# Performance work log

Hardware: AMD Instinct MI355X
Metric: run time of the kernel (lower is better)

The kernel has to match this reference:

```python
import jax, jax.numpy as jnp
import numpy as np

C = 64
EPS = 1e-5

def _layernorm(x, w, b):
    mu = jnp.mean(x, axis=-1, keepdims=True)
    var = jnp.var(x, axis=-1, keepdims=True)
    return (x - mu) * jax.lax.rsqrt(var + EPS) * w + b

def setup_inputs() -> dict:
    key = jax.random.key(0)
    ks = jax.random.split(key, 12)
    B, H, W = 4, 64, 64
    s = 1.0 / np.sqrt(C)
    inp = {
        'seg':   jax.random.normal(ks[0], (B, C, H, W), jnp.float32),
        'gauss': jax.random.normal(ks[1], (B, C, H, W), jnp.float32),
        'Wq': jax.random.normal(ks[2], (C, C), jnp.float32) * s,
        'bq': jnp.zeros((C,), jnp.float32),
        'Wk': jax.random.normal(ks[3], (C, C), jnp.float32) * s,
        'bk': jnp.zeros((C,), jnp.float32),
        'Wv': jax.random.normal(ks[4], (C, C), jnp.float32) * s,
        'bv': jnp.zeros((C,), jnp.float32),
        'ln1_w': jnp.ones((C,), jnp.float32),
        'ln1_b': jnp.zeros((C,), jnp.float32),
        'ln2_w': jnp.ones((C,), jnp.float32),
        'ln2_b': jnp.zeros((C,), jnp.float32),
        'W1': jax.random.normal(ks[5], (C, C), jnp.float32) * s,
        'b1': jnp.zeros((C,), jnp.float32),
        'W2': jax.random.normal(ks[6], (C, C), jnp.float32) * s,
        'b2': jnp.zeros((C,), jnp.float32),
    }
    return inp

def reference(seg, gauss, Wq, bq, Wk, bk, Wv, bv, ln1_w, ln1_b, ln2_w, ln2_b, W1, b1, W2, b2):
    B, Cc, H, W_ = seg.shape
    N = H * W_
    # 1x1 convs == per-pixel linear over channels; go straight to token layout
    seg_t = seg.reshape(B, Cc, N)      # [B,C,N]
    gau_t = gauss.reshape(B, Cc, N)
    q = jnp.einsum('bcn,oc->bno', seg_t, Wq) + bq        # [B,N,C]
    k = jnp.einsum('bcn,oc->bon', seg_t, Wk) + bk[None, :, None]  # [B,C,N]
    v = jnp.einsum('bcn,oc->bno', gau_t, Wv) + bv        # [B,N,C]
    scale = 1.0 / jnp.sqrt(jnp.float32(Cc))
    attn = jax.nn.softmax(jnp.einsum('bnc,bcm->bnm', q, k) * scale, axis=-1)  # [B,N,N]
    out = jnp.einsum('bnm,bmc->bnc', attn, v)
    x = _layernorm(v + out, ln1_w, ln1_b)
    ffn = jnp.einsum('bnc,oc->bno', jax.nn.relu(jnp.einsum('bnc,oc->bno', x, W1) + b1), W2) + b2
    x = _layernorm(x + ffn, ln2_w, ln2_b)
    return x.transpose(0, 2, 1).reshape(B, Cc, H, W_)
```

## Files before the change

kernel.cpp:

```cpp
#include <hip/hip_runtime.h>
#include <hip/hip_bf16.h>

typedef unsigned short u16;
typedef unsigned int u32;
typedef __attribute__((ext_vector_type(8))) short bf16x8;
typedef __attribute__((ext_vector_type(4))) float f32x4;

#define NTOK 4096
#define QSCALE2 0.18033688f

__device__ __forceinline__ float b2f(u16 u) {
    u32 v = ((u32)u) << 16;
    return __builtin_bit_cast(float, v);
}
__device__ __forceinline__ u16 f2b(float f) {
    u32 u = __builtin_bit_cast(u32, f);
    u32 r = (u + 0x7fffu + ((u >> 16) & 1u)) >> 16;
    return (u16)r;
}
__device__ __forceinline__ u32 pack2(float lo, float hi) {
    return (u32)f2b(lo) | ((u32)f2b(hi) << 16);
}
__device__ __forceinline__ u32 pk2(float lo, float hi) {
    float2 t; t.x = lo; t.y = hi;
    __hip_bfloat162 b = __float22bfloat162_rn(t);
    u32 r;
    __builtin_memcpy(&r, &b, 4);
    return r;
}
__device__ __forceinline__ bf16x8 cvt8(const float* __restrict__ p) {
    float4 a = *(const float4*)p;
    float4 b = *(const float4*)(p + 4);
    bf16x8 r;
    r[0] = (short)f2b(a.x); r[1] = (short)f2b(a.y);
    r[2] = (short)f2b(a.z); r[3] = (short)f2b(a.w);
    r[4] = (short)f2b(b.x); r[5] = (short)f2b(b.y);
    r[6] = (short)f2b(b.z); r[7] = (short)f2b(b.w);
    return r;
}

__global__ __launch_bounds__(512) void qkv_kernel(
    const float* __restrict__ seg, const float* __restrict__ gau,
    const float* __restrict__ Wq, const float* __restrict__ bq,
    const float* __restrict__ Wk, const float* __restrict__ bk,
    const float* __restrict__ Wv, const float* __restrict__ bv,
    u16* __restrict__ Qt, u16* __restrict__ Kt,
    u16* __restrict__ Vtok, u16* __restrict__ Vswz)
{
    __shared__ __align__(16) u16 sSegT[64 * 64];
    __shared__ __align__(16) u16 sGauT[64 * 64];
    const int tid = threadIdx.x;
    const int bid = blockIdx.x;
    const int xcd = bid & 7;
    const int b = xcd >> 1;
    const int nb = ((bid >> 3) << 1) | (xcd & 1);
    const int n0 = nb * 64;

    for (int idx = tid; idx < 4096; idx += 512) {
        int c = idx >> 6, t = idx & 63;
        int sw = t * 64 + ((((c >> 3) ^ (t & 7)) << 3) | (c & 7));
        sSegT[sw] = f2b(seg[(size_t)(b * 64 + c) * NTOK + n0 + t]);
        sGauT[sw] = f2b(gau[(size_t)(b * 64 + c) * NTOK + n0 + t]);
    }
    __syncthreads();

    const int lane = tid & 63;
    const int wv = tid >> 6;
    const int tb = wv & 3;
    const int task = wv >> 2;
    const int q = lane & 15, g = lane >> 4;
    const int tok = tb * 16 + q;

    const size_t obase = (size_t)b * NTOK * 64;
    const size_t rowb = (size_t)(n0 + tb * 16 + g * 4);

    if (task == 0) {
        bf16x8 as[2];
#pragma unroll
        for (int ks = 0; ks < 2; ++ks) {
            int c0 = ks * 32 + g * 8;
            int sw = tok * 64 + (((c0 >> 3) ^ (tok & 7)) << 3);
            as[ks] = *(const bf16x8*)&sSegT[sw];
        }
#pragma unroll
        for (int ob = 0; ob < 4; ++ob) {
            int o = ob * 16 + q;
            {
                float bias = bq[o];
                f32x4 acc = {bias, bias, bias, bias};
                bf16x8 w0 = cvt8(&Wq[o * 64 + g * 8]);
                bf16x8 w1 = cvt8(&Wq[o * 64 + 32 + g * 8]);
                acc = __builtin_amdgcn_mfma_f32_16x16x32_bf16(as[0], w0, acc, 0, 0, 0);
                acc = __builtin_amdgcn_mfma_f32_16x16x32_bf16(as[1], w1, acc, 0, 0, 0);
#pragma unroll
                for (int j = 0; j < 4; ++j)
                    Qt[obase + (rowb + j) * 64 + o] = f2b(acc[j] * QSCALE2);
            }
            {
                float bias = bk[o];
                f32x4 acc = {bias, bias, bias, bias};
                bf16x8 w0 = cvt8(&Wk[o * 64 + g * 8]);
                bf16x8 w1 = cvt8(&Wk[o * 64 + 32 + g * 8]);
                acc = __builtin_amdgcn_mfma_f32_16x16x32_bf16(as[0], w0, acc, 0, 0, 0);
                acc = __builtin_amdgcn_mfma_f32_16x16x32_bf16(as[1], w1, acc, 0, 0, 0);
#pragma unroll
                for (int j = 0; j < 4; ++j)
                    Kt[obase + (rowb + j) * 64 + o] = f2b(acc[j]);
            }
        }
    } else {
        bf16x8 ag[2];
#pragma unroll
        for (int ks = 0; ks < 2; ++ks) {
            int c0 = ks * 32 + g * 8;
            int sw = tok * 64 + (((c0 >> 3) ^ (tok & 7)) << 3);
            ag[ks] = *(const bf16x8*)&sGauT[sw];
        }
        const int kbg = (n0 >> 5) + (tb >> 1);
        const int half = tb & 1;
#pragma unroll
        for (int ob = 0; ob < 4; ++ob) {
            int o = ob * 16 + q;
            float bias = bv[o];
            f32x4 acc = {bias, bias, bias, bias};
            bf16x8 w0 = cvt8(&Wv[o * 64 + g * 8]);
            bf16x8 w1 = cvt8(&Wv[o * 64 + 32 + g * 8]);
            acc = __builtin_amdgcn_mfma_f32_16x16x32_bf16(ag[0], w0, acc, 0, 0, 0);
            acc = __builtin_amdgcn_mfma_f32_16x16x32_bf16(ag[1], w1, acc, 0, 0, 0);
            ushort4 v4;
            v4.x = f2b(acc[0]); v4.y = f2b(acc[1]);
            v4.z = f2b(acc[2]); v4.w = f2b(acc[3]);
#pragma unroll
            for (int j = 0; j < 4; ++j)
                Vtok[obase + (rowb + j) * 64 + o] = f2b(acc[j]);
            *(ushort4*)&Vswz[(((size_t)(b * 128 + kbg)) * 4 + ob) * 512 + lane * 8 + half * 4] = v4;
        }
    }
}

__global__ __launch_bounds__(512, 4) void attn_kernel(
    const u16* __restrict__ Qt, const u16* __restrict__ Kt,
    const u16* __restrict__ Vtok, const u16* __restrict__ Vswz,
    const float* __restrict__ ln1w, const float* __restrict__ ln1b,
    const float* __restrict__ ln2w, const float* __restrict__ ln2b,
    const float* __restrict__ W1, const float* __restrict__ b1,
    const float* __restrict__ W2, const float* __restrict__ b2,
    float* __restrict__ out)
{
    __shared__ __align__(16) float sAcc[4][32][68];
    __shared__ float sL[8][32];
    __shared__ __align__(16) u16 sX[2 * 16 * 64];

    const int tid = threadIdx.x;
    const int wv = tid >> 6;
    const int lane = tid & 63;
    const int q = lane & 15, g = lane >> 4;
    const int bid = blockIdx.x;
    const int xcd = bid & 7;
    const int b = xcd >> 1;
    const int qb = ((bid >> 3) << 1) | (xcd & 1);
    const int q0 = qb * 32;
    const size_t tb_ = (size_t)b * NTOK * 64;

    const int n_qa = q0 + q, n_qb = q0 + 16 + q;
    bf16x8 qa0 = *(const bf16x8*)&Qt[tb_ + (size_t)n_qa * 64 + g * 8];
    bf16x8 qa1 = *(const bf16x8*)&Qt[tb_ + (size_t)n_qa * 64 + 32 + g * 8];
    bf16x8 qb0 = *(const bf16x8*)&Qt[tb_ + (size_t)n_qb * 64 + g * 8];
    bf16x8 qb1 = *(const bf16x8*)&Qt[tb_ + (size_t)n_qb * 64 + 32 + g * 8];

    f32x4 zero4 = {0.f, 0.f, 0.f, 0.f};
    f32x4 acc_a[4], acc_b[4];
#pragma unroll
    for (int i = 0; i < 4; ++i) { acc_a[i] = zero4; acc_b[i] = zero4; }
    float l_a = 0.f, l_b = 0.f;

    const int kbeg = wv * 512;
    const u16* Kp = &Kt[tb_ + (size_t)kbeg * 64];
    const u16* Vsw = Vswz + ((size_t)(b * 128 + (kbeg >> 5)) * 4) * 512 + lane * 8;

    for (int kk = 0; kk < 512; kk += 32) {
        bf16x8 kf00 = *(const bf16x8*)&Kp[q * 64 + g * 8];
        bf16x8 kf01 = *(const bf16x8*)&Kp[q * 64 + 32 + g * 8];
        bf16x8 kf10 = *(const bf16x8*)&Kp[(16 + q) * 64 + g * 8];
        bf16x8 kf11 = *(const bf16x8*)&Kp[(16 + q) * 64 + 32 + g * 8];
        Kp += 32 * 64;

        const u16* vt = Vsw + (size_t)(kk >> 5) * 4 * 512;
        bf16x8 vf0 = *(const bf16x8*)&vt[0 * 512];
        bf16x8 vf1 = *(const bf16x8*)&vt[1 * 512];
        bf16x8 vf2 = *(const bf16x8*)&vt[2 * 512];
        bf16x8 vf3 = *(const bf16x8*)&vt[3 * 512];

        f32x4 s0a = __builtin_amdgcn_mfma_f32_16x16x32_bf16(kf00, qa0, zero4, 0, 0, 0);
        s0a = __builtin_amdgcn_mfma_f32_16x16x32_bf16(kf01, qa1, s0a, 0, 0, 0);
        f32x4 s1a = __builtin_amdgcn_mfma_f32_16x16x32_bf16(kf10, qa0, zero4, 0, 0, 0);
        s1a = __builtin_amdgcn_mfma_f32_16x16x32_bf16(kf11, qa1, s1a, 0, 0, 0);
        f32x4 s0b = __builtin_amdgcn_mfma_f32_16x16x32_bf16(kf00, qb0, zero4, 0, 0, 0);
        s0b = __builtin_amdgcn_mfma_f32_16x16x32_bf16(kf01, qb1, s0b, 0, 0, 0);
        f32x4 s1b = __builtin_amdgcn_mfma_f32_16x16x32_bf16(kf10, qb0, zero4, 0, 0, 0);
        s1b = __builtin_amdgcn_mfma_f32_16x16x32_bf16(kf11, qb1, s1b, 0, 0, 0);

        {
            float p0 = __builtin_exp2f(s0a[0]);
            float p1 = __builtin_exp2f(s0a[1]);
            float p2 = __builtin_exp2f(s0a[2]);
            float p3 = __builtin_exp2f(s0a[3]);
            float p4 = __builtin_exp2f(s1a[0]);
            float p5 = __builtin_exp2f(s1a[1]);
            float p6 = __builtin_exp2f(s1a[2]);
            float p7 = __builtin_exp2f(s1a[3]);
            l_a += ((p0 + p1) + (p2 + p3)) + ((p4 + p5) + (p6 + p7));
            u32 pwv[4] = {pk2(p0, p1), pk2(p2, p3), pk2(p4, p5), pk2(p6, p7)};
            bf16x8 pf = __builtin_bit_cast(bf16x8, *(const bf16x8*)pwv);
            acc_a[0] = __builtin_amdgcn_mfma_f32_16x16x32_bf16(vf0, pf, acc_a[0], 0, 0, 0);
            acc_a[1] = __builtin_amdgcn_mfma_f32_16x16x32_bf16(vf1, pf, acc_a[1], 0, 0, 0);
            acc_a[2] = __builtin_amdgcn_mfma_f32_16x16x32_bf16(vf2, pf, acc_a[2], 0, 0, 0);
            acc_a[3] = __builtin_amdgcn_mfma_f32_16x16x32_bf16(vf3, pf, acc_a[3], 0, 0, 0);
        }
        {
            float p0 = __builtin_exp2f(s0b[0]);
            float p1 = __builtin_exp2f(s0b[1]);
            float p2 = __builtin_exp2f(s0b[2]);
            float p3 = __builtin_exp2f(s0b[3]);
            float p4 = __builtin_exp2f(s1b[0]);
            float p5 = __builtin_exp2f(s1b[1]);
            float p6 = __builtin_exp2f(s1b[2]);
            float p7 = __builtin_exp2f(s1b[3]);
            l_b += ((p0 + p1) + (p2 + p3)) + ((p4 + p5) + (p6 + p7));
            u32 pwv[4] = {pk2(p0, p1), pk2(p2, p3), pk2(p4, p5), pk2(p6, p7)};
            bf16x8 pf = __builtin_bit_cast(bf16x8, *(const bf16x8*)pwv);
            acc_b[0] = __builtin_amdgcn_mfma_f32_16x16x32_bf16(vf0, pf, acc_b[0], 0, 0, 0);
            acc_b[1] = __builtin_amdgcn_mfma_f32_16x16x32_bf16(vf1, pf, acc_b[1], 0, 0, 0);
            acc_b[2] = __builtin_amdgcn_mfma_f32_16x16x32_bf16(vf2, pf, acc_b[2], 0, 0, 0);
            acc_b[3] = __builtin_amdgcn_mfma_f32_16x16x32_bf16(vf3, pf, acc_b[3], 0, 0, 0);
        }
    }

    l_a += __shfl_xor(l_a, 16); l_a += __shfl_xor(l_a, 32);
    l_b += __shfl_xor(l_b, 16); l_b += __shfl_xor(l_b, 32);

    if (wv >= 4) {
        const int s = wv - 4;
        sL[wv][q] = l_a;      sL[wv][16 + q] = l_b;
#pragma unroll
        for (int cb = 0; cb < 4; ++cb) {
            *(f32x4*)&sAcc[s][q][cb * 16 + g * 4] = acc_a[cb];
            *(f32x4*)&sAcc[s][16 + q][cb * 16 + g * 4] = acc_b[cb];
        }
    }
    __syncthreads();

    if (wv < 4) {
        l_a += sL[wv + 4][q];
        l_b += sL[wv + 4][16 + q];
#pragma unroll
        for (int cb = 0; cb < 4; ++cb) {
            f32x4 pa = *(const f32x4*)&sAcc[wv][q][cb * 16 + g * 4];
            f32x4 pb = *(const f32x4*)&sAcc[wv][16 + q][cb * 16 + g * 4];
#pragma unroll
            for (int j = 0; j < 4; ++j) {
                acc_a[cb][j] += pa[j];
                acc_b[cb][j] += pb[j];
            }
        }
        sL[wv][q] = l_a;      sL[wv][16 + q] = l_b;
#pragma unroll
        for (int cb = 0; cb < 4; ++cb) {
            *(f32x4*)&sAcc[wv][q][cb * 16 + g * 4] = acc_a[cb];
            *(f32x4*)&sAcc[wv][16 + q][cb * 16 + g * 4] = acc_b[cb];
        }
    }
    __syncthreads();
    if (wv >= 2) return;

    const int qe = wv * 16 + q;
    const int n_q = q0 + qe;

    float L = sL[0][qe] + sL[1][qe] + sL[2][qe] + sL[3][qe];
    f32x4 o[4];
#pragma unroll
    for (int cb = 0; cb < 4; ++cb) o[cb] = zero4;
#pragma unroll
    for (int w = 0; w < 4; ++w) {
#pragma unroll
        for (int cb = 0; cb < 4; ++cb) {
            f32x4 aw = *(const f32x4*)&sAcc[w][qe][cb * 16 + g * 4];
#pragma unroll
            for (int j = 0; j < 4; ++j) o[cb][j] += aw[j];
        }
    }

    float inv_l = 1.0f / L;
    float x1[4][4];
#pragma unroll
    for (int cb = 0; cb < 4; ++cb) {
        ushort4 vv = *(const ushort4*)&Vtok[tb_ + (size_t)n_q * 64 + cb * 16 + g * 4];
        x1[cb][0] = o[cb][0] * inv_l + b2f(vv.x);
        x1[cb][1] = o[cb][1] * inv_l + b2f(vv.y);
        x1[cb][2] = o[cb][2] * inv_l + b2f(vv.z);
        x1[cb][3] = o[cb][3] * inv_l + b2f(vv.w);
    }

    float s_ = 0.f;
#pragma unroll
    for (int cb = 0; cb < 4; ++cb)
        for (int j = 0; j < 4; ++j) s_ += x1[cb][j];
    s_ += __shfl_xor(s_, 16); s_ += __shfl_xor(s_, 32);
    float mean = s_ * (1.f / 64.f);
    float v_ = 0.f;
#pragma unroll
    for (int cb = 0; cb < 4; ++cb)
        for (int j = 0; j < 4; ++j) { float d = x1[cb][j] - mean; v_ += d * d; }
    v_ += __shfl_xor(v_, 16); v_ += __shfl_xor(v_, 32);
    float rstd = rsqrtf(v_ * (1.f / 64.f) + 1e-5f);

    float xh[4][4];
#pragma unroll
    for (int cb = 0; cb < 4; ++cb) {
        float4 lw = *(const float4*)&ln1w[cb * 16 + g * 4];
        float4 lb = *(const float4*)&ln1b[cb * 16 + g * 4];
        xh[cb][0] = (x1[cb][0] - mean) * rstd * lw.x + lb.x;
        xh[cb][1] = (x1[cb][1] - mean) * rstd * lw.y + lb.y;
        xh[cb][2] = (x1[cb][2] - mean) * rstd * lw.z + lb.z;
        xh[cb][3] = (x1[cb][3] - mean) * rstd * lw.w + lb.w;
    }

    u32* sXu = (u32*)sX;
    const int xwr = wv * 512 + q * 32;
#pragma unroll
    for (int cb = 0; cb < 4; ++cb) {
        sXu[xwr + cb * 8 + g * 2 + 0] = pack2(xh[cb][0], xh[cb][1]);
        sXu[xwr + cb * 8 + g * 2 + 1] = pack2(xh[cb][2], xh[cb][3]);
    }
    asm volatile("s_waitcnt lgkmcnt(0)" ::: "memory");
    __builtin_amdgcn_sched_barrier(0);
    const u16* xrp = &sX[wv * 1024 + q * 64 + g * 8];
    bf16x8 xb0 = *(const bf16x8*)&xrp[0];
    bf16x8 xb1 = *(const bf16x8*)&xrp[32];

    float h[4][4];
#pragma unroll
    for (int ob = 0; ob < 4; ++ob) {
        float4 bb = *(const float4*)&b1[ob * 16 + g * 4];
        f32x4 hacc = {bb.x, bb.y, bb.z, bb.w};
        bf16x8 w0 = cvt8(&W1[(size_t)(ob * 16 + q) * 64 + g * 8]);
        bf16x8 w1 = cvt8(&W1[(size_t)(ob * 16 + q) * 64 + 32 + g * 8]);
        hacc = __builtin_amdgcn_mfma_f32_16x16x32_bf16(w0, xb0, hacc, 0, 0, 0);
        hacc = __builtin_amdgcn_mfma_f32_16x16x32_bf16(w1, xb1, hacc, 0, 0, 0);
#pragma unroll
        for (int j = 0; j < 4; ++j) h[ob][j] = fmaxf(hacc[j], 0.f);
    }

#pragma unroll
    for (int ob = 0; ob < 4; ++ob) {
        sXu[xwr + ob * 8 + g * 2 + 0] = pack2(h[ob][0], h[ob][1]);
        sXu[xwr + ob * 8 + g * 2 + 1] = pack2(h[ob][2], h[ob][3]);
    }
    asm volatile("s_waitcnt lgkmcnt(0)" ::: "memory");
    __builtin_amdgcn_sched_barrier(0);
    bf16x8 hb0 = *(const bf16x8*)&xrp[0];
    bf16x8 hb1 = *(const bf16x8*)&xrp[32];

    float f_[4][4];
#pragma unroll
    for (int cb = 0; cb < 4; ++cb) {
        float4 bb = *(const float4*)&b2[cb * 16 + g * 4];
        f32x4 yacc = {bb.x, bb.y, bb.z, bb.w};
        bf16x8 w0 = cvt8(&W2[(size_t)(cb * 16 + q) * 64 + g * 8]);
        bf16x8 w1 = cvt8(&W2[(size_t)(cb * 16 + q) * 64 + 32 + g * 8]);
        yacc = __builtin_amdgcn_mfma_f32_16x16x32_bf16(w0, hb0, yacc, 0, 0, 0);
        yacc = __builtin_amdgcn_mfma_f32_16x16x32_bf16(w1, hb1, yacc, 0, 0, 0);
#pragma unroll
        for (int j = 0; j < 4; ++j) f_[cb][j] = xh[cb][j] + yacc[j];
    }

    float s2 = 0.f;
#pragma unroll
    for (int cb = 0; cb < 4; ++cb)
        for (int j = 0; j < 4; ++j) s2 += f_[cb][j];
    s2 += __shfl_xor(s2, 16); s2 += __shfl_xor(s2, 32);
    float mean2 = s2 * (1.f / 64.f);
    float v2 = 0.f;
#pragma unroll
    for (int cb = 0; cb < 4; ++cb)
        for (int j = 0; j < 4; ++j) { float d = f_[cb][j] - mean2; v2 += d * d; }
    v2 += __shfl_xor(v2, 16); v2 += __shfl_xor(v2, 32);
    float rstd2 = rsqrtf(v2 * (1.f / 64.f) + 1e-5f);

#pragma unroll
    for (int cb = 0; cb < 4; ++cb) {
        float4 lw = *(const float4*)&ln2w[cb * 16 + g * 4];
        float4 lb = *(const float4*)&ln2b[cb * 16 + g * 4];
        float o0 = (f_[cb][0] - mean2) * rstd2 * lw.x + lb.x;
        float o1 = (f_[cb][1] - mean2) * rstd2 * lw.y + lb.y;
        float o2 = (f_[cb][2] - mean2) * rstd2 * lw.z + lb.z;
        float o3 = (f_[cb][3] - mean2) * rstd2 * lw.w + lb.w;
        out[(size_t)(b * 64 + cb * 16 + g * 4 + 0) * NTOK + n_q] = o0;
        out[(size_t)(b * 64 + cb * 16 + g * 4 + 1) * NTOK + n_q] = o1;
        out[(size_t)(b * 64 + cb * 16 + g * 4 + 2) * NTOK + n_q] = o2;
        out[(size_t)(b * 64 + cb * 16 + g * 4 + 3) * NTOK + n_q] = o3;
    }
}

extern "C" void kernel_launch(void* const* d_in, const int* in_sizes, int n_in,
                              void* d_out, int out_size, void* d_ws, size_t ws_size,
                              hipStream_t stream) {
    const float* seg = (const float*)d_in[0];
    const float* gau = (const float*)d_in[1];
    const float* Wq = (const float*)d_in[2];
    const float* bq = (const float*)d_in[3];
    const float* Wk = (const float*)d_in[4];
    const float* bk = (const float*)d_in[5];
    const float* Wv = (const float*)d_in[6];
    const float* bv = (const float*)d_in[7];
    const float* ln1w = (const float*)d_in[8];
    const float* ln1b = (const float*)d_in[9];
    const float* ln2w = (const float*)d_in[10];
    const float* ln2b = (const float*)d_in[11];
    const float* W1 = (const float*)d_in[12];
    const float* b1 = (const float*)d_in[13];
    const float* W2 = (const float*)d_in[14];
    const float* b2 = (const float*)d_in[15];

    u16* Qt = (u16*)d_ws;
    u16* Kt = Qt + (size_t)4 * NTOK * 64;
    u16* Vtok = Kt + (size_t)4 * NTOK * 64;
    u16* Vswz = Vtok + (size_t)4 * NTOK * 64;
    float* outp = (float*)d_out;

    hipLaunchKernelGGL(qkv_kernel, dim3(256), dim3(512), 0, stream,
                       seg, gau, Wq, bq, Wk, bk, Wv, bv, Qt, Kt, Vtok, Vswz);
    hipLaunchKernelGGL(attn_kernel, dim3(512), dim3(512), 0, stream,
                       Qt, Kt, Vtok, Vswz, ln1w, ln1b, ln2w, ln2b,
                       W1, b1, W2, b2, outp);
}
```

Measured before the change: 63.77 us.

## Prestage K in MFMA fragment layout and double-buffer K/V via global_load_lds

The QKV kernel now writes K into a fragment-swizzled layout (through an LDS staging buffer) that matches the V swizzle, so the attention kernel can read both with contiguous 16-byte per-lane chunks. The attention loop issues asynchronous global-to-LDS loads for the next K/V tile into a per-wave double buffer while computing on the current tile, to hide global load latency. The partial-sum scratch is aliased onto the same LDS region after a vmcnt wait, and launch bounds drop the occupancy hint from 4 to 2 blocks per CU, which risks lower occupancy given the much larger LDS footprint (~128KB). No explicit wait is placed before each LDS read of the freshly loaded tile, which may rely on implicit ordering.

New measurement: 59.58 us. 6.6% less time.

```diff
diff --git a/kernel.cpp b/kernel.cpp
--- a/kernel.cpp
+++ b/kernel.cpp
@@ -8,6 +8,10 @@
 
 #define NTOK 4096
 #define QSCALE2 0.18033688f
+
+#define GLD_LDS(g, l) __builtin_amdgcn_global_load_lds( \
+    (const __attribute__((address_space(1))) void*)(g), \
+    (__attribute__((address_space(3))) void*)(l), 16, 0, 0)
 
 __device__ __forceinline__ float b2f(u16 u) {
     u32 v = ((u32)u) << 16;
@@ -44,11 +48,12 @@
     const float* __restrict__ Wq, const float* __restrict__ bq,
     const float* __restrict__ Wk, const float* __restrict__ bk,
     const float* __restrict__ Wv, const float* __restrict__ bv,
-    u16* __restrict__ Qt, u16* __restrict__ Kt,
+    u16* __restrict__ Qt, u16* __restrict__ Kfrag,
     u16* __restrict__ Vtok, u16* __restrict__ Vswz)
 {
     __shared__ __align__(16) u16 sSegT[64 * 64];
     __shared__ __align__(16) u16 sGauT[64 * 64];
+    __shared__ __align__(16) u16 kBuf[64 * 64];
     const int tid = threadIdx.x;
     const int bid = blockIdx.x;
     const int xcd = bid & 7;
@@ -105,7 +110,7 @@
                 acc = __builtin_amdgcn_mfma_f32_16x16x32_bf16(as[1], w1, acc, 0, 0, 0);
 #pragma unroll
                 for (int j = 0; j < 4; ++j)
-                    Kt[obase + (rowb + j) * 64 + o] = f2b(acc[j]);
+                    kBuf[(tb * 16 + g * 4 + j) * 64 + o] = f2b(acc[j]);
             }
         }
     } else {
@@ -136,10 +141,22 @@
             *(ushort4*)&Vswz[(((size_t)(b * 128 + kbg)) * 4 + ob) * 512 + lane * 8 + half * 4] = v4;
         }
     }
-}
-
-__global__ __launch_bounds__(512, 4) void attn_kernel(
-    const u16* __restrict__ Qt, const u16* __restrict__ Kt,
+    __syncthreads();
+
+    {
+        const int F = (wv * 64 + lane) * 8;
+        const int kb2 = F >> 11;
+        const int f = (F >> 9) & 3;
+        const int l2 = (F >> 3) & 63;
+        const int R = kb2 * 32 + ((f >> 1) << 4) + (l2 & 15);
+        const int c0 = ((f & 1) << 5) + ((l2 >> 4) << 3);
+        bf16x8 v = *(const bf16x8*)&kBuf[R * 64 + c0];
+        *(bf16x8*)&Kfrag[(((size_t)(b * 128 + nb * 2 + kb2)) * 4 + f) * 512 + l2 * 8] = v;
+    }
+}
+
+__global__ __launch_bounds__(512, 2) void attn_kernel(
+    const u16* __restrict__ Qt, const u16* __restrict__ Kfrag,
     const u16* __restrict__ Vtok, const u16* __restrict__ Vswz,
     const float* __restrict__ ln1w, const float* __restrict__ ln1b,
     const float* __restrict__ ln2w, const float* __restrict__ ln2b,
@@ -147,9 +164,9 @@
     const float* __restrict__ W2, const float* __restrict__ b2,
     float* __restrict__ out)
 {
-    __shared__ __align__(16) float sAcc[4][32][68];
+    __shared__ __align__(16) u16 smem[8 * 2 * 4096];
+    __shared__ __align__(16) u16 sX[2 * 16 * 64];
     __shared__ float sL[8][32];
-    __shared__ __align__(16) u16 sX[2 * 16 * 64];
 
     const int tid = threadIdx.x;
     const int wv = tid >> 6;
@@ -175,21 +192,40 @@
     float l_a = 0.f, l_b = 0.f;
 
     const int kbeg = wv * 512;
-    const u16* Kp = &Kt[tb_ + (size_t)kbeg * 64];
-    const u16* Vsw = Vswz + ((size_t)(b * 128 + (kbeg >> 5)) * 4) * 512 + lane * 8;
-
-    for (int kk = 0; kk < 512; kk += 32) {
-        bf16x8 kf00 = *(const bf16x8*)&Kp[q * 64 + g * 8];
-        bf16x8 kf01 = *(const bf16x8*)&Kp[q * 64 + 32 + g * 8];
-        bf16x8 kf10 = *(const bf16x8*)&Kp[(16 + q) * 64 + g * 8];
-        bf16x8 kf11 = *(const bf16x8*)&Kp[(16 + q) * 64 + 32 + g * 8];
-        Kp += 32 * 64;
-
-        const u16* vt = Vsw + (size_t)(kk >> 5) * 4 * 512;
-        bf16x8 vf0 = *(const bf16x8*)&vt[0 * 512];
-        bf16x8 vf1 = *(const bf16x8*)&vt[1 * 512];
-        bf16x8 vf2 = *(const bf16x8*)&vt[2 * 512];
-        bf16x8 vf3 = *(const bf16x8*)&vt[3 * 512];
+    const size_t kvb = ((size_t)(b * 128 + (kbeg >> 5))) * 2048;
+    const u16* gK = Kfrag + kvb + lane * 8;
+    const u16* gV = Vswz + kvb + lane * 8;
+    u16* stW = &smem[wv * 8192];
+    u16* lK = stW + lane * 8;
+
+#pragma unroll
+    for (int i = 0; i < 4; ++i) GLD_LDS(gK + i * 512, lK + i * 512);
+#pragma unroll
+    for (int i = 0; i < 4; ++i) GLD_LDS(gV + i * 512, lK + 2048 + i * 512);
+
+    for (int it = 0; it < 16; ++it) {
+        const int cur = it & 1;
+        const u16* sb = &stW[cur * 4096];
+        bf16x8 kf00 = *(const bf16x8*)&sb[0 * 512 + lane * 8];
+        bf16x8 kf01 = *(const bf16x8*)&sb[1 * 512 + lane * 8];
+        bf16x8 kf10 = *(const bf16x8*)&sb[2 * 512 + lane * 8];
+        bf16x8 kf11 = *(const bf16x8*)&sb[3 * 512 + lane * 8];
+        bf16x8 vf0 = *(const bf16x8*)&sb[2048 + 0 * 512 + lane * 8];
+        bf16x8 vf1 = *(const bf16x8*)&sb[2048 + 1 * 512 + lane * 8];
+        bf16x8 vf2 = *(const bf16x8*)&sb[2048 + 2 * 512 + lane * 8];
+        bf16x8 vf3 = *(const bf16x8*)&sb[2048 + 3 * 512 + lane * 8];
+
+        {
+            const int tn = (it < 15) ? it + 1 : 15;
+            const u16* gk = gK + (size_t)tn * 2048;
+            const u16* gv = gV + (size_t)tn * 2048;
+            u16* lk = lK + (cur ^ 1) * 4096;
+#pragma unroll
+            for (int i = 0; i < 4; ++i) GLD_LDS(gk + i * 512, lk + i * 512);
+#pragma unroll
+            for (int i = 0; i < 4; ++i) GLD_LDS(gv + i * 512, lk + 2048 + i * 512);
+        }
+        __builtin_amdgcn_sched_barrier(0);
 
         f32x4 s0a = __builtin_amdgcn_mfma_f32_16x16x32_bf16(kf00, qa0, zero4, 0, 0, 0);
         s0a = __builtin_amdgcn_mfma_f32_16x16x32_bf16(kf01, qa1, s0a, 0, 0, 0);
@@ -239,13 +275,18 @@
     l_a += __shfl_xor(l_a, 16); l_a += __shfl_xor(l_a, 32);
     l_b += __shfl_xor(l_b, 16); l_b += __shfl_xor(l_b, 32);
 
+    asm volatile("s_waitcnt vmcnt(0)" ::: "memory");
+    __syncthreads();
+    float* sAcc = (float*)smem;
+#define SACC(w_, r_) (&sAcc[(((w_) * 32) + (r_)) * 68])
+
     if (wv >= 4) {
         const int s = wv - 4;
         sL[wv][q] = l_a;      sL[wv][16 + q] = l_b;
 #pragma unroll
         for (int cb = 0; cb < 4; ++cb) {
-            *(f32x4*)&sAcc[s][q][cb * 16 + g * 4] = acc_a[cb];
-            *(f32x4*)&sAcc[s][16 + q][cb * 16 + g * 4] = acc_b[cb];
+            *(f32x4*)&SACC(s, q)[cb * 16 + g * 4] = acc_a[cb];
+            *(f32x4*)&SACC(s, 16 + q)[cb * 16 + g * 4] = acc_b[cb];
         }
     }
     __syncthreads();
@@ -255,8 +296,8 @@
         l_b += sL[wv + 4][16 + q];
 #pragma unroll
         for (int cb = 0; cb < 4; ++cb) {
-            f32x4 pa = *(const f32x4*)&sAcc[wv][q][cb * 16 + g * 4];
-            f32x4 pb = *(const f32x4*)&sAcc[wv][16 + q][cb * 16 + g * 4];
+            f32x4 pa = *(const f32x4*)&SACC(wv, q)[cb * 16 + g * 4];
+            f32x4 pb = *(const f32x4*)&SACC(wv, 16 + q)[cb * 16 + g * 4];
 #pragma unroll
             for (int j = 0; j < 4; ++j) {
                 acc_a[cb][j] += pa[j];
@@ -266,8 +307,8 @@
         sL[wv][q] = l_a;      sL[wv][16 + q] = l_b;
 #pragma unroll
         for (int cb = 0; cb < 4; ++cb) {
-            *(f32x4*)&sAcc[wv][q][cb * 16 + g * 4] = acc_a[cb];
-            *(f32x4*)&sAcc[wv][16 + q][cb * 16 + g * 4] = acc_b[cb];
+            *(f32x4*)&SACC(wv, q)[cb * 16 + g * 4] = acc_a[cb];
+            *(f32x4*)&SACC(wv, 16 + q)[cb * 16 + g * 4] = acc_b[cb];
         }
     }
     __syncthreads();
@@ -284,7 +325,7 @@
     for (int w = 0; w < 4; ++w) {
 #pragma unroll
         for (int cb = 0; cb < 4; ++cb) {
-            f32x4 aw = *(const f32x4*)&sAcc[w][qe][cb * 16 + g * 4];
+            f32x4 aw = *(const f32x4*)&SACC(w, qe)[cb * 16 + g * 4];
 #pragma unroll
             for (int j = 0; j < 4; ++j) o[cb][j] += aw[j];
         }
@@ -423,14 +464,14 @@
     const float* b2 = (const float*)d_in[15];
 
     u16* Qt = (u16*)d_ws;
-    u16* Kt = Qt + (size_t)4 * NTOK * 64;
-    u16* Vtok = Kt + (size_t)4 * NTOK * 64;
+    u16* Kfrag = Qt + (size_t)4 * NTOK * 64;
+    u16* Vtok = Kfrag + (size_t)4 * NTOK * 64;
     u16* Vswz = Vtok + (size_t)4 * NTOK * 64;
     float* outp = (float*)d_out;
 
     hipLaunchKernelGGL(qkv_kernel, dim3(256), dim3(512), 0, stream,
-                       seg, gau, Wq, bq, Wk, bk, Wv, bv, Qt, Kt, Vtok, Vswz);
+                       seg, gau, Wq, bq, Wk, bk, Wv, bv, Qt, Kfrag, Vtok, Vswz);
     hipLaunchKernelGGL(attn_kernel, dim3(512), dim3(512), 0, stream,
-                       Qt, Kt, Vtok, Vswz, ln1w, ln1b, ln2w, ln2b,
+                       Qt, Kfrag, Vtok, Vswz, ln1w, ln1b, ln2w, ln2b,
                        W1, b1, W2, b2, outp);
 }
```
